# Optimization experiments

Hardware: AMD Instinct MI355X
Metric: run time of the kernel (lower is better)

Reference implementation:

```python
import jax, jax.numpy as jnp
import numpy as np

N_NODES = 50000
D = 512
N_EDGES = 1600000

def setup_inputs() -> dict:
    key = jax.random.key(0)
    ks = jax.random.split(key, 5)
    x = jax.random.normal(ks[0], (N_NODES, D), dtype=jnp.float32)
    W = jax.random.normal(ks[1], (D, D), dtype=jnp.float32) * (1.0 / np.sqrt(D))
    b = jnp.zeros((D,), dtype=jnp.float32)
    edge_weight = jax.random.uniform(ks[2], (N_EDGES,), dtype=jnp.float32)
    edge_src = jax.random.randint(ks[3], (N_EDGES,), 0, N_NODES, dtype=jnp.int32)
    edge_dst = jax.random.randint(ks[4], (N_EDGES,), 0, N_NODES, dtype=jnp.int32)
    return {"x": x, "W": W, "b": b, "edge_weight": edge_weight,
            "edge_src": edge_src, "edge_dst": edge_dst}

def reference(x, W, b, edge_weight, edge_src, edge_dst):
    # GraphConvolution: support = x @ W; out = spmm(adj, support) + b
    support = x @ W                                  # [N, D] dense GEMM
    msgs = support[edge_src] * edge_weight[:, None]  # gather + scale [E, D]
    agg = jax.ops.segment_sum(msgs, edge_dst, num_segments=x.shape[0])  # [N, D]
    gc_out = agg + b
    # GCN2: relu then residual
    return jax.nn.relu(gc_out) + x
```

## Files before the change

### kernel.cpp

```cpp
#include <hip/hip_runtime.h>

#define N_NODES 50000
#define DIM 512
#define KCAT 1024
#define N_EDGES 1600000
#define CAP 96

typedef __attribute__((ext_vector_type(8))) short short8;
typedef __attribute__((ext_vector_type(8))) unsigned short ushort8;
typedef __attribute__((ext_vector_type(4))) float floatx4;
typedef __attribute__((ext_vector_type(2))) unsigned int uintx2;

__device__ __forceinline__ unsigned short f2bf(float v) {
    unsigned u = __float_as_uint(v);
    unsigned r = u + 0x7FFF + ((u >> 16) & 1);
    return (unsigned short)(r >> 16);
}
__device__ __forceinline__ float bf2f(unsigned short h) {
    return __uint_as_float((unsigned)h << 16);
}
__device__ __forceinline__ void stage16(const char* g, char* l) {
    __builtin_amdgcn_global_load_lds((const __attribute__((address_space(1))) void*)g,
                                     (__attribute__((address_space(3))) void*)l, 16, 0, 0);
}

__global__ __launch_bounds__(256) void convert_x(const float* __restrict__ x,
                                                 unsigned short* __restrict__ xcat) {
    const int t = blockIdx.x * 256 + threadIdx.x;
    if (t >= N_NODES * 64) return;
    const int row = t >> 6;
    const int kc = t & 63;
    const int blk = kc >> 3;
    const int c = kc & 7;
    const int cSw = c ^ (row & 7);

    const floatx4 v0 = __builtin_nontemporal_load((const floatx4*)&x[row * DIM + kc * 8]);
    const floatx4 v1 = __builtin_nontemporal_load((const floatx4*)&x[row * DIM + kc * 8 + 4]);
    float v[8] = {v0.x, v0.y, v0.z, v0.w, v1.x, v1.y, v1.z, v1.w};
    unsigned short h[8], l[8];
#pragma unroll
    for (int j = 0; j < 8; j++) {
        h[j] = f2bf(v[j]);
        l[j] = f2bf(v[j] - bf2f(h[j]));
    }
    const int o = row * KCAT + blk * 64 + cSw * 8;
    *(short8*)&xcat[o] = *(short8*)h;
    *(short8*)&xcat[o + DIM] = *(short8*)l;
}

__global__ __launch_bounds__(256) void convert_w(const float* __restrict__ W,
                                                 unsigned short* __restrict__ wcat) {
    const int t = blockIdx.x * 256 + threadIdx.x;
    if (t >= DIM * 64) return;
    const int n = t >> 6;
    const int kc = t & 63;
    const int blk = kc >> 3;
    const int c = kc & 7;
    const int cSw = c ^ (n & 7);

    unsigned short h[8];
#pragma unroll
    for (int j = 0; j < 8; j++) h[j] = f2bf(W[(kc * 8 + j) * DIM + n]);
    const int o = n * KCAT + blk * 64 + cSw * 8;
    *(short8*)&wcat[o] = *(short8*)h;
    *(short8*)&wcat[o + DIM] = *(short8*)h;
}

__global__ __launch_bounds__(256, 3) void gemm_cat(const unsigned short* __restrict__ A,
                                                   const unsigned short* __restrict__ B,
                                                   unsigned short* __restrict__ Cb, int M) {
    __shared__ __align__(128) char smem[32768];

    const int tid = threadIdx.x;
    const int row0 = blockIdx.y * 128;
    const int col0 = blockIdx.x * 128;

    int srow[4], schk[4];
#pragma unroll
    for (int i = 0; i < 4; i++) {
        const int q = i * 256 + tid;
        srow[i] = q >> 3;
        schk[i] = q & 7;
    }

    const int l = tid & 63;
    const int w = tid >> 6;
    const int wm = w & 1, wn = w >> 1;
    const int lrow = l & 15;
    const int kg = l >> 4;
    const int s = l & 7;

    int offA[4][2], offB[4][2];
#pragma unroll
    for (int mt = 0; mt < 4; mt++)
#pragma unroll
        for (int h = 0; h < 2; h++) {
            const int chunk = (kg + 4 * h) ^ s;
            offA[mt][h] = (wm * 64 + mt * 16 + lrow) * 128 + chunk * 16;
            offB[mt][h] = 16384 + (wn * 64 + mt * 16 + lrow) * 128 + chunk * 16;
        }

    floatx4 acc[4][4];
#pragma unroll
    for (int i = 0; i < 4; i++)
#pragma unroll
        for (int j = 0; j < 4; j++) acc[i][j] = (floatx4)(0.f);

    const char* A8 = (const char*)A;
    const char* B8 = (const char*)B;

    for (int kblk = 0; kblk < 16; kblk++) {
        __syncthreads();
#pragma unroll
        for (int i = 0; i < 4; i++) {
            const int q16 = (i * 256 + tid) * 16;
            const size_t ga = (size_t)min(row0 + srow[i], M - 1) * (KCAT * 2)
                              + kblk * 128 + schk[i] * 16;
            const size_t gb = (size_t)(col0 + srow[i]) * (KCAT * 2)
                              + kblk * 128 + schk[i] * 16;
            stage16(A8 + ga, smem + q16);
            stage16(B8 + gb, smem + 16384 + q16);
        }
        __syncthreads();

#pragma unroll
        for (int h = 0; h < 2; h++) {
            short8 bf[4];
#pragma unroll
            for (int nt = 0; nt < 4; nt++) bf[nt] = *(const short8*)(smem + offB[nt][h]);
#pragma unroll
            for (int mt = 0; mt < 4; mt++) {
                const short8 af = *(const short8*)(smem + offA[mt][h]);
#pragma unroll
                for (int nt = 0; nt < 4; nt++)
                    acc[mt][nt] = __builtin_amdgcn_mfma_f32_16x16x32_bf16(
                        af, bf[nt], acc[mt][nt], 0, 0, 0);
            }
        }
    }

    const int crow0 = row0 + wm * 64;
    const int ccol0 = col0 + wn * 64;
#pragma unroll
    for (int mt = 0; mt < 4; mt++) {
        const int rbase = crow0 + mt * 16 + kg * 4;
#pragma unroll
        for (int nt = 0; nt < 4; nt++) {
            const int cc = ccol0 + nt * 16 + lrow;
#pragma unroll
            for (int r = 0; r < 4; r++) {
                const int gr = rbase + r;
                if (gr < M) Cb[(size_t)gr * DIM + cc] = f2bf(acc[mt][nt][r]);
            }
        }
    }
}

__global__ __launch_bounds__(256) void gcn_build_edges(const int* __restrict__ esrc,
                                                       const int* __restrict__ edst,
                                                       const float* __restrict__ ew,
                                                       int* __restrict__ cursor,
                                                       unsigned int* __restrict__ table) {
    const int e = blockIdx.x * 256 + threadIdx.x;
    if (e >= N_EDGES) return;
    const int d = __builtin_nontemporal_load(&edst[e]);
    const int s = __builtin_nontemporal_load(&esrc[e]);
    const float w = __builtin_nontemporal_load(&ew[e]);
    const int pos = atomicAdd(&cursor[d], 1);
    if (pos < CAP) {
        uintx2 pk;
        pk.x = (unsigned)s;
        pk.y = __float_as_uint(w);
        __builtin_nontemporal_store(pk, (uintx2*)&table[(size_t)(d * CAP + pos) * 2]);
    }
}

__global__ __launch_bounds__(64, 8) void gcn_aggregate(const unsigned short* __restrict__ sup,
                                                       const int* __restrict__ cursor,
                                                       const unsigned int* __restrict__ table,
                                                       const unsigned short* __restrict__ xcat,
                                                       const float* __restrict__ b,
                                                       float* __restrict__ out) {
    const int n = blockIdx.x;
    const int tid = threadIdx.x;
    const int c = tid * 8;

    __shared__ uintx2 s_e[CAP];
    const int deg = min(cursor[n], CAP);
    if (tid < deg)
        s_e[tid] = __builtin_nontemporal_load((const uintx2*)&table[(size_t)(n * CAP + tid) * 2]);
    if (tid + 64 < deg)
        s_e[tid + 64] = __builtin_nontemporal_load((const uintx2*)&table[(size_t)(n * CAP + tid + 64) * 2]);
    __syncthreads();

    float acc[8];
#pragma unroll
    for (int j = 0; j < 8; j++) acc[j] = 0.f;

    const unsigned short* supc = sup + c;

    int i = 0;
    for (; i + 8 <= deg; i += 8) {
        float wts[8];
        ushort8 v[8];
#pragma unroll
        for (int u = 0; u < 8; u++) {
            const uintx2 e = s_e[i + u];
            wts[u] = __uint_as_float(e.y);
            v[u] = *(const ushort8*)(supc + (size_t)e.x * DIM);
        }
#pragma unroll
        for (int u = 0; u < 8; u++)
#pragma unroll
            for (int j = 0; j < 8; j++) acc[j] = fmaf(wts[u], bf2f(v[u][j]), acc[j]);
    }
    for (; i < deg; i++) {
        const uintx2 e = s_e[i];
        const float wt = __uint_as_float(e.y);
        const ushort8 v = *(const ushort8*)(supc + (size_t)e.x * DIM);
#pragma unroll
        for (int j = 0; j < 8; j++) acc[j] = fmaf(wt, bf2f(v[j]), acc[j]);
    }

    const int xoff = n * KCAT + (tid >> 3) * 64 + (((tid & 7) ^ (n & 7)) * 8);
    const ushort8 xb = __builtin_nontemporal_load((const ushort8*)&xcat[xoff]);
    const float4 b0 = *(const float4*)&b[c];
    const float4 b1 = *(const float4*)&b[c + 4];
    const float bb[8] = {b0.x, b0.y, b0.z, b0.w, b1.x, b1.y, b1.z, b1.w};
    floatx4 o0, o1;
    float o[8];
#pragma unroll
    for (int j = 0; j < 8; j++) o[j] = fmaxf(acc[j] + bb[j], 0.f) + bf2f(xb[j]);
    o0.x = o[0]; o0.y = o[1]; o0.z = o[2]; o0.w = o[3];
    o1.x = o[4]; o1.y = o[5]; o1.z = o[6]; o1.w = o[7];
    __builtin_nontemporal_store(o0, (floatx4*)&out[n * DIM + c]);
    __builtin_nontemporal_store(o1, (floatx4*)&out[n * DIM + c + 4]);
}

extern "C" void kernel_launch(void* const* d_in, const int* in_sizes, int n_in,
                              void* d_out, int out_size, void* d_ws, size_t ws_size,
                              hipStream_t stream) {
    const float* x = (const float*)d_in[0];
    const float* W = (const float*)d_in[1];
    const float* b = (const float*)d_in[2];
    const float* ew = (const float*)d_in[3];
    const int* esrc = (const int*)d_in[4];
    const int* edst = (const int*)d_in[5];
    float* out = (float*)d_out;

    char* ws = (char*)d_ws;
    size_t off = 0;
    unsigned short* support = (unsigned short*)(ws + off); off += (size_t)N_NODES * DIM * 2;
    int* cursor = (int*)(ws + off);                   off += (size_t)N_NODES * 4;
    unsigned int* table = (unsigned int*)(ws + off);  off += (size_t)N_NODES * CAP * 8;
    unsigned short* xcat = (unsigned short*)(ws + off); off += (size_t)N_NODES * KCAT * 2;
    unsigned short* wcat = (unsigned short*)(ws + off); off += (size_t)DIM * KCAT * 2;

    (void)hipMemsetAsync(cursor, 0, (size_t)N_NODES * sizeof(int), stream);

    convert_w<<<(DIM * 64 + 255) / 256, 256, 0, stream>>>(W, wcat);
    convert_x<<<(N_NODES * 64 + 255) / 256, 256, 0, stream>>>(x, xcat);

    gcn_build_edges<<<(N_EDGES + 255) / 256, 256, 0, stream>>>(esrc, edst, ew,
                                                               cursor, table);

    dim3 gemm_grid(DIM / 128, (N_NODES + 127) / 128);
    gemm_cat<<<gemm_grid, 256, 0, stream>>>(xcat, wcat, support, N_NODES);

    gcn_aggregate<<<N_NODES, 64, 0, stream>>>(support, cursor, table, xcat, b, out);
}
```

Before: 645.2 us.

## Bucket edges by source chunk and aggregate eight destinations per block

Replaces the single atomic edge-bucketing pass with a count, prefix and scatter sequence. Edges are now ordered within each destination by source chunk of 2048 nodes. The aggregation kernel handles eight destination nodes per 64-thread block and walks the chunks in order, so gathers of support rows from the same source range happen close together in time, aiming for better cache reuse. In exchange it adds an extra pass over the edges and a larger bounds array to clear, and the inner gather loop is no longer unrolled, which leaves fewer independent loads in flight per wave. CAP also drops from 96 to 80, which raises the risk of dropping edges at high-degree nodes.

```diff
diff --git a/kernel.cpp b/kernel.cpp
--- a/kernel.cpp
+++ b/kernel.cpp
@@ -4,7 +4,10 @@
 #define DIM 512
 #define KCAT 1024
 #define N_EDGES 1600000
-#define CAP 96
+#define CAP 80
+#define CHSHIFT 11
+#define NCHUNK 25
+#define DPW 8
 
 typedef __attribute__((ext_vector_type(8))) short short8;
 typedef __attribute__((ext_vector_type(8))) unsigned short ushort8;
@@ -156,17 +159,39 @@
     }
 }
 
-__global__ __launch_bounds__(256) void gcn_build_edges(const int* __restrict__ esrc,
-                                                       const int* __restrict__ edst,
-                                                       const float* __restrict__ ew,
-                                                       int* __restrict__ cursor,
-                                                       unsigned int* __restrict__ table) {
+__global__ __launch_bounds__(256) void gcn_count(const int* __restrict__ esrc,
+                                                 const int* __restrict__ edst,
+                                                 int* __restrict__ bounds) {
     const int e = blockIdx.x * 256 + threadIdx.x;
     if (e >= N_EDGES) return;
+    const int s = __builtin_nontemporal_load(&esrc[e]);
     const int d = __builtin_nontemporal_load(&edst[e]);
+    atomicAdd(&bounds[(s >> CHSHIFT) * N_NODES + d], 1);
+}
+
+__global__ __launch_bounds__(256) void gcn_prefix(int* __restrict__ bounds) {
+    const int dst = blockIdx.x * 256 + threadIdx.x;
+    if (dst >= N_NODES) return;
+    int run = 0;
+#pragma unroll
+    for (int c = 0; c < NCHUNK; c++) {
+        const int t = bounds[c * N_NODES + dst];
+        bounds[c * N_NODES + dst] = run;
+        run += t;
+    }
+}
+
+__global__ __launch_bounds__(256) void gcn_scatter(const int* __restrict__ esrc,
+                                                   const int* __restrict__ edst,
+                                                   const float* __restrict__ ew,
+                                                   int* __restrict__ bounds,
+                                                   unsigned int* __restrict__ table) {
+    const int e = blockIdx.x * 256 + threadIdx.x;
+    if (e >= N_EDGES) return;
     const int s = __builtin_nontemporal_load(&esrc[e]);
+    const int d = __builtin_nontemporal_load(&edst[e]);
     const float w = __builtin_nontemporal_load(&ew[e]);
-    const int pos = atomicAdd(&cursor[d], 1);
+    const int pos = atomicAdd(&bounds[(s >> CHSHIFT) * N_NODES + d], 1);
     if (pos < CAP) {
         uintx2 pk;
         pk.x = (unsigned)s;
@@ -175,66 +200,61 @@
     }
 }
 
-__global__ __launch_bounds__(64, 8) void gcn_aggregate(const unsigned short* __restrict__ sup,
-                                                       const int* __restrict__ cursor,
+__global__ __launch_bounds__(64, 4) void gcn_aggregate(const unsigned short* __restrict__ sup,
+                                                       const int* __restrict__ bounds,
                                                        const unsigned int* __restrict__ table,
                                                        const unsigned short* __restrict__ xcat,
                                                        const float* __restrict__ b,
                                                        float* __restrict__ out) {
-    const int n = blockIdx.x;
+    const int nb = blockIdx.x * DPW;
     const int tid = threadIdx.x;
-    const int c = tid * 8;
-
-    __shared__ uintx2 s_e[CAP];
-    const int deg = min(cursor[n], CAP);
-    if (tid < deg)
-        s_e[tid] = __builtin_nontemporal_load((const uintx2*)&table[(size_t)(n * CAP + tid) * 2]);
-    if (tid + 64 < deg)
-        s_e[tid + 64] = __builtin_nontemporal_load((const uintx2*)&table[(size_t)(n * CAP + tid + 64) * 2]);
-    __syncthreads();
-
-    float acc[8];
-#pragma unroll
-    for (int j = 0; j < 8; j++) acc[j] = 0.f;
-
-    const unsigned short* supc = sup + c;
-
-    int i = 0;
-    for (; i + 8 <= deg; i += 8) {
-        float wts[8];
-        ushort8 v[8];
-#pragma unroll
-        for (int u = 0; u < 8; u++) {
-            const uintx2 e = s_e[i + u];
-            wts[u] = __uint_as_float(e.y);
-            v[u] = *(const ushort8*)(supc + (size_t)e.x * DIM);
-        }
-#pragma unroll
-        for (int u = 0; u < 8; u++)
-#pragma unroll
-            for (int j = 0; j < 8; j++) acc[j] = fmaf(wts[u], bf2f(v[u][j]), acc[j]);
-    }
-    for (; i < deg; i++) {
-        const uintx2 e = s_e[i];
-        const float wt = __uint_as_float(e.y);
-        const ushort8 v = *(const ushort8*)(supc + (size_t)e.x * DIM);
-#pragma unroll
-        for (int j = 0; j < 8; j++) acc[j] = fmaf(wt, bf2f(v[j]), acc[j]);
-    }
-
-    const int xoff = n * KCAT + (tid >> 3) * 64 + (((tid & 7) ^ (n & 7)) * 8);
-    const ushort8 xb = __builtin_nontemporal_load((const ushort8*)&xcat[xoff]);
-    const float4 b0 = *(const float4*)&b[c];
-    const float4 b1 = *(const float4*)&b[c + 4];
+    const int c8 = tid * 8;
+
+    float acc[DPW][8];
+#pragma unroll
+    for (int d = 0; d < DPW; d++)
+#pragma unroll
+        for (int j = 0; j < 8; j++) acc[d][j] = 0.f;
+
+    int prevEnd[DPW];
+#pragma unroll
+    for (int d = 0; d < DPW; d++) prevEnd[d] = 0;
+
+    const unsigned short* supc = sup + c8;
+
+    for (int c = 0; c < NCHUNK; c++) {
+#pragma unroll
+        for (int d = 0; d < DPW; d++) {
+            const int dst = nb + d;
+            const int end = min(bounds[c * N_NODES + dst], CAP);
+            for (int i = prevEnd[d]; i < end; i++) {
+                const uintx2 e = *(const uintx2*)&table[(size_t)(dst * CAP + i) * 2];
+                const float wt = __uint_as_float(e.y);
+                const ushort8 v = *(const ushort8*)(supc + (size_t)e.x * DIM);
+#pragma unroll
+                for (int j = 0; j < 8; j++) acc[d][j] = fmaf(wt, bf2f(v[j]), acc[d][j]);
+            }
+            prevEnd[d] = end;
+        }
+    }
+
+    const float4 b0 = *(const float4*)&b[c8];
+    const float4 b1 = *(const float4*)&b[c8 + 4];
     const float bb[8] = {b0.x, b0.y, b0.z, b0.w, b1.x, b1.y, b1.z, b1.w};
-    floatx4 o0, o1;
-    float o[8];
-#pragma unroll
-    for (int j = 0; j < 8; j++) o[j] = fmaxf(acc[j] + bb[j], 0.f) + bf2f(xb[j]);
-    o0.x = o[0]; o0.y = o[1]; o0.z = o[2]; o0.w = o[3];
-    o1.x = o[4]; o1.y = o[5]; o1.z = o[6]; o1.w = o[7];
-    __builtin_nontemporal_store(o0, (floatx4*)&out[n * DIM + c]);
-    __builtin_nontemporal_store(o1, (floatx4*)&out[n * DIM + c + 4]);
+#pragma unroll
+    for (int d = 0; d < DPW; d++) {
+        const int n = nb + d;
+        const int xoff = n * KCAT + (tid >> 3) * 64 + (((tid & 7) ^ (n & 7)) * 8);
+        const ushort8 xb = __builtin_nontemporal_load((const ushort8*)&xcat[xoff]);
+        float o[8];
+#pragma unroll
+        for (int j = 0; j < 8; j++) o[j] = fmaxf(acc[d][j] + bb[j], 0.f) + bf2f(xb[j]);
+        floatx4 o0, o1;
+        o0.x = o[0]; o0.y = o[1]; o0.z = o[2]; o0.w = o[3];
+        o1.x = o[4]; o1.y = o[5]; o1.z = o[6]; o1.w = o[7];
+        __builtin_nontemporal_store(o0, (floatx4*)&out[(size_t)n * DIM + c8]);
+        __builtin_nontemporal_store(o1, (floatx4*)&out[(size_t)n * DIM + c8 + 4]);
+    }
 }
 
 extern "C" void kernel_launch(void* const* d_in, const int* in_sizes, int n_in,
@@ -251,21 +271,22 @@
     char* ws = (char*)d_ws;
     size_t off = 0;
     unsigned short* support = (unsigned short*)(ws + off); off += (size_t)N_NODES * DIM * 2;
-    int* cursor = (int*)(ws + off);                   off += (size_t)N_NODES * 4;
+    int* bounds = (int*)(ws + off);                   off += (size_t)NCHUNK * N_NODES * 4;
     unsigned int* table = (unsigned int*)(ws + off);  off += (size_t)N_NODES * CAP * 8;
     unsigned short* xcat = (unsigned short*)(ws + off); off += (size_t)N_NODES * KCAT * 2;
     unsigned short* wcat = (unsigned short*)(ws + off); off += (size_t)DIM * KCAT * 2;
 
-    (void)hipMemsetAsync(cursor, 0, (size_t)N_NODES * sizeof(int), stream);
+    (void)hipMemsetAsync(bounds, 0, (size_t)NCHUNK * N_NODES * sizeof(int), stream);
 
     convert_w<<<(DIM * 64 + 255) / 256, 256, 0, stream>>>(W, wcat);
     convert_x<<<(N_NODES * 64 + 255) / 256, 256, 0, stream>>>(x, xcat);
 
-    gcn_build_edges<<<(N_EDGES + 255) / 256, 256, 0, stream>>>(esrc, edst, ew,
-                                                               cursor, table);
+    gcn_count<<<(N_EDGES + 255) / 256, 256, 0, stream>>>(esrc, edst, bounds);
+    gcn_prefix<<<(N_NODES + 255) / 256, 256, 0, stream>>>(bounds);
+    gcn_scatter<<<(N_EDGES + 255) / 256, 256, 0, stream>>>(esrc, edst, ew, bounds, table);
 
     dim3 gemm_grid(DIM / 128, (N_NODES + 127) / 128);
     gemm_cat<<<gemm_grid, 256, 0, stream>>>(xcat, wcat, support, N_NODES);
 
-    gcn_aggregate<<<N_NODES, 64, 0, stream>>>(support, cursor, table, xcat, b, out);
-}
+    gcn_aggregate<<<N_NODES / DPW, 64, 0, stream>>>(support, bounds, table, xcat, b, out);
+}
```

Result: slower. 767.9 us (+19.0%).

## Sort per-node edge lists by source and stagger gather start for cache locality

Applied to the files above, without the earlier changes.

Each aggregation block now bitonic-sorts its edge list by source index in shared memory, then starts its gather at a source offset that depends on the node id and wraps around. The aim is for concurrently running blocks to touch similar regions of the support matrix at the same time, improving L2 hit rates for the random gathers. The cost is a 28-step shared-memory sort with a barrier per step, and the loop loses its batched 8-wide load unrolling, which reduces memory-level parallelism.

```diff
diff --git a/kernel.cpp b/kernel.cpp
--- a/kernel.cpp
+++ b/kernel.cpp
@@ -5,6 +5,7 @@
 #define KCAT 1024
 #define N_EDGES 1600000
 #define CAP 96
+#define GEN 6400
 
 typedef __attribute__((ext_vector_type(8))) short short8;
 typedef __attribute__((ext_vector_type(8))) unsigned short ushort8;
@@ -175,57 +176,75 @@
     }
 }
 
-__global__ __launch_bounds__(64, 8) void gcn_aggregate(const unsigned short* __restrict__ sup,
-                                                       const int* __restrict__ cursor,
-                                                       const unsigned int* __restrict__ table,
-                                                       const unsigned short* __restrict__ xcat,
-                                                       const float* __restrict__ b,
-                                                       float* __restrict__ out) {
+__global__ __launch_bounds__(64) void gcn_aggregate(const unsigned short* __restrict__ sup,
+                                                    const int* __restrict__ cursor,
+                                                    const unsigned int* __restrict__ table,
+                                                    const unsigned short* __restrict__ xcat,
+                                                    const float* __restrict__ b,
+                                                    float* __restrict__ out) {
     const int n = blockIdx.x;
     const int tid = threadIdx.x;
-    const int c = tid * 8;
-
-    __shared__ uintx2 s_e[CAP];
+    const int c8 = tid * 8;
+
+    __shared__ uintx2 s_e[128];
     const int deg = min(cursor[n], CAP);
-    if (tid < deg)
-        s_e[tid] = __builtin_nontemporal_load((const uintx2*)&table[(size_t)(n * CAP + tid) * 2]);
-    if (tid + 64 < deg)
-        s_e[tid + 64] = __builtin_nontemporal_load((const uintx2*)&table[(size_t)(n * CAP + tid + 64) * 2]);
+
+    uintx2 pad; pad.x = 0xFFFFFFFFu; pad.y = 0;
+    s_e[tid] = (tid < deg)
+        ? *(const uintx2*)&table[(size_t)(n * CAP + tid) * 2] : pad;
+    s_e[tid + 64] = (tid + 64 < deg)
+        ? *(const uintx2*)&table[(size_t)(n * CAP + tid + 64) * 2] : pad;
     __syncthreads();
 
+#pragma unroll
+    for (int k = 2; k <= 128; k <<= 1) {
+        for (int j = k >> 1; j > 0; j >>= 1) {
+            const int i = ((tid & ~(j - 1)) << 1) | (tid & (j - 1));
+            const int p = i | j;
+            const uintx2 a = s_e[i];
+            const uintx2 q = s_e[p];
+            const bool up = (i & k) == 0;
+            const bool sw = up ? (a.x > q.x) : (a.x < q.x);
+            if (sw) { s_e[i] = q; s_e[p] = a; }
+            __syncthreads();
+        }
+    }
+
+    const unsigned s0 =
+        (unsigned)(((unsigned long long)(n % GEN) * N_NODES) / GEN);
+    const unsigned long long m0 = __ballot(s_e[tid].x >= s0);
+    const unsigned long long m1 = __ballot(s_e[tid + 64].x >= s0);
+    int start = m0 ? (__ffsll((long long)m0) - 1)
+                   : (m1 ? 64 + __ffsll((long long)m1) - 1 : 128);
+    start = min(start, deg);
+
     float acc[8];
 #pragma unroll
     for (int j = 0; j < 8; j++) acc[j] = 0.f;
 
-    const unsigned short* supc = sup + c;
-
-    int i = 0;
-    for (; i + 8 <= deg; i += 8) {
-        float wts[8];
-        ushort8 v[8];
-#pragma unroll
-        for (int u = 0; u < 8; u++) {
-            const uintx2 e = s_e[i + u];
-            wts[u] = __uint_as_float(e.y);
-            v[u] = *(const ushort8*)(supc + (size_t)e.x * DIM);
-        }
-#pragma unroll
-        for (int u = 0; u < 8; u++)
-#pragma unroll
-            for (int j = 0; j < 8; j++) acc[j] = fmaf(wts[u], bf2f(v[u][j]), acc[j]);
-    }
-    for (; i < deg; i++) {
+    const unsigned short* supc = sup + c8;
+
+#pragma unroll 4
+    for (int i = start; i < deg; i++) {
         const uintx2 e = s_e[i];
         const float wt = __uint_as_float(e.y);
         const ushort8 v = *(const ushort8*)(supc + (size_t)e.x * DIM);
 #pragma unroll
         for (int j = 0; j < 8; j++) acc[j] = fmaf(wt, bf2f(v[j]), acc[j]);
     }
+#pragma unroll 4
+    for (int i = 0; i < start; i++) {
+        const uintx2 e = s_e[i];
+        const float wt = __uint_as_float(e.y);
+        const ushort8 v = *(const ushort8*)(supc + (size_t)e.x * DIM);
+#pragma unroll
+        for (int j = 0; j < 8; j++) acc[j] = fmaf(wt, bf2f(v[j]), acc[j]);
+    }
 
     const int xoff = n * KCAT + (tid >> 3) * 64 + (((tid & 7) ^ (n & 7)) * 8);
     const ushort8 xb = __builtin_nontemporal_load((const ushort8*)&xcat[xoff]);
-    const float4 b0 = *(const float4*)&b[c];
-    const float4 b1 = *(const float4*)&b[c + 4];
+    const float4 b0 = *(const float4*)&b[c8];
+    const float4 b1 = *(const float4*)&b[c8 + 4];
     const float bb[8] = {b0.x, b0.y, b0.z, b0.w, b1.x, b1.y, b1.z, b1.w};
     floatx4 o0, o1;
     float o[8];
@@ -233,8 +252,8 @@
     for (int j = 0; j < 8; j++) o[j] = fmaxf(acc[j] + bb[j], 0.f) + bf2f(xb[j]);
     o0.x = o[0]; o0.y = o[1]; o0.z = o[2]; o0.w = o[3];
     o1.x = o[4]; o1.y = o[5]; o1.z = o[6]; o1.w = o[7];
-    __builtin_nontemporal_store(o0, (floatx4*)&out[n * DIM + c]);
-    __builtin_nontemporal_store(o1, (floatx4*)&out[n * DIM + c + 4]);
+    __builtin_nontemporal_store(o0, (floatx4*)&out[n * DIM + c8]);
+    __builtin_nontemporal_store(o1, (floatx4*)&out[n * DIM + c8 + 4]);
 }
 
 extern "C" void kernel_launch(void* const* d_in, const int* in_sizes, int n_in,
```

New measurement: 631.3 us. 2.2% less time.

## Bucket edges by source chunk and sweep chunks across destinations in persistent aggregate

Applied to the files above, without the earlier changes.

Edges are now binned per destination into four source-index chunks (by src>>14), each capped at 40 slots. A persistent aggregate kernel gives each wave 12 destination nodes and walks chunk by chunk across all of them. At any moment the gathered support rows come from one quarter of the node range, which should improve L2 hit rate on the random gathers. A tail kernel handles the leftover nodes. In exchange, each wave holds 96 float accumulators per lane with lower occupancy, the edge list is no longer staged in LDS, and per-chunk caps could drop edges for skewed degree distributions.

```diff
diff --git a/kernel.cpp b/kernel.cpp
--- a/kernel.cpp
+++ b/kernel.cpp
@@ -4,7 +4,11 @@
 #define DIM 512
 #define KCAT 1024
 #define N_EDGES 1600000
-#define CAP 96
+#define NCHUNK 4
+#define CAPC 40
+#define PBLK 4096
+#define DPW 12
+#define TAIL (N_NODES - PBLK * DPW)
 
 typedef __attribute__((ext_vector_type(8))) short short8;
 typedef __attribute__((ext_vector_type(8))) unsigned short ushort8;
@@ -166,75 +170,112 @@
     const int d = __builtin_nontemporal_load(&edst[e]);
     const int s = __builtin_nontemporal_load(&esrc[e]);
     const float w = __builtin_nontemporal_load(&ew[e]);
-    const int pos = atomicAdd(&cursor[d], 1);
-    if (pos < CAP) {
+    const int ch = s >> 14;
+    const int pos = atomicAdd(&cursor[ch * N_NODES + d], 1);
+    if (pos < CAPC) {
         uintx2 pk;
         pk.x = (unsigned)s;
         pk.y = __float_as_uint(w);
-        __builtin_nontemporal_store(pk, (uintx2*)&table[(size_t)(d * CAP + pos) * 2]);
-    }
-}
-
-__global__ __launch_bounds__(64, 8) void gcn_aggregate(const unsigned short* __restrict__ sup,
-                                                       const int* __restrict__ cursor,
-                                                       const unsigned int* __restrict__ table,
-                                                       const unsigned short* __restrict__ xcat,
-                                                       const float* __restrict__ b,
-                                                       float* __restrict__ out) {
-    const int n = blockIdx.x;
-    const int tid = threadIdx.x;
-    const int c = tid * 8;
-
-    __shared__ uintx2 s_e[CAP];
-    const int deg = min(cursor[n], CAP);
-    if (tid < deg)
-        s_e[tid] = __builtin_nontemporal_load((const uintx2*)&table[(size_t)(n * CAP + tid) * 2]);
-    if (tid + 64 < deg)
-        s_e[tid + 64] = __builtin_nontemporal_load((const uintx2*)&table[(size_t)(n * CAP + tid + 64) * 2]);
-    __syncthreads();
-
-    float acc[8];
-#pragma unroll
-    for (int j = 0; j < 8; j++) acc[j] = 0.f;
-
-    const unsigned short* supc = sup + c;
-
-    int i = 0;
-    for (; i + 8 <= deg; i += 8) {
-        float wts[8];
-        ushort8 v[8];
-#pragma unroll
-        for (int u = 0; u < 8; u++) {
-            const uintx2 e = s_e[i + u];
-            wts[u] = __uint_as_float(e.y);
-            v[u] = *(const ushort8*)(supc + (size_t)e.x * DIM);
-        }
-#pragma unroll
-        for (int u = 0; u < 8; u++)
-#pragma unroll
-            for (int j = 0; j < 8; j++) acc[j] = fmaf(wts[u], bf2f(v[u][j]), acc[j]);
-    }
-    for (; i < deg; i++) {
-        const uintx2 e = s_e[i];
-        const float wt = __uint_as_float(e.y);
-        const ushort8 v = *(const ushort8*)(supc + (size_t)e.x * DIM);
-#pragma unroll
-        for (int j = 0; j < 8; j++) acc[j] = fmaf(wt, bf2f(v[j]), acc[j]);
-    }
-
+        __builtin_nontemporal_store(
+            pk, (uintx2*)&table[(((size_t)d * NCHUNK + ch) * CAPC + pos) * 2]);
+    }
+}
+
+__device__ __forceinline__ void write_node(int n, int tid, const float* acc,
+                                           const float* bb,
+                                           const unsigned short* __restrict__ xcat,
+                                           float* __restrict__ out) {
+    const int c8 = tid * 8;
     const int xoff = n * KCAT + (tid >> 3) * 64 + (((tid & 7) ^ (n & 7)) * 8);
     const ushort8 xb = __builtin_nontemporal_load((const ushort8*)&xcat[xoff]);
-    const float4 b0 = *(const float4*)&b[c];
-    const float4 b1 = *(const float4*)&b[c + 4];
-    const float bb[8] = {b0.x, b0.y, b0.z, b0.w, b1.x, b1.y, b1.z, b1.w};
+    float o[8];
+#pragma unroll
+    for (int j = 0; j < 8; j++) o[j] = fmaxf(acc[j] + bb[j], 0.f) + bf2f(xb[j]);
     floatx4 o0, o1;
-    float o[8];
-#pragma unroll
-    for (int j = 0; j < 8; j++) o[j] = fmaxf(acc[j] + bb[j], 0.f) + bf2f(xb[j]);
     o0.x = o[0]; o0.y = o[1]; o0.z = o[2]; o0.w = o[3];
     o1.x = o[4]; o1.y = o[5]; o1.z = o[6]; o1.w = o[7];
-    __builtin_nontemporal_store(o0, (floatx4*)&out[n * DIM + c]);
-    __builtin_nontemporal_store(o1, (floatx4*)&out[n * DIM + c + 4]);
+    __builtin_nontemporal_store(o0, (floatx4*)&out[(size_t)n * DIM + c8]);
+    __builtin_nontemporal_store(o1, (floatx4*)&out[(size_t)n * DIM + c8 + 4]);
+}
+
+__global__ __launch_bounds__(64, 4) void gcn_aggregate_pers(
+        const unsigned short* __restrict__ sup,
+        const int* __restrict__ cursor,
+        const unsigned int* __restrict__ table,
+        const unsigned short* __restrict__ xcat,
+        const float* __restrict__ b,
+        float* __restrict__ out) {
+    const int w = blockIdx.x;
+    const int tid = threadIdx.x;
+    const int c8 = tid * 8;
+
+    float acc[DPW][8];
+#pragma unroll
+    for (int k = 0; k < DPW; k++)
+#pragma unroll
+        for (int j = 0; j < 8; j++) acc[k][j] = 0.f;
+
+    const unsigned short* supc = sup + c8;
+
+    for (int c = 0; c < NCHUNK; c++) {
+#pragma unroll
+        for (int k = 0; k < DPW; k++) {
+            const int dst = w + k * PBLK;
+            const int cnt = min(cursor[c * N_NODES + dst], CAPC);
+            const size_t segbase = ((size_t)dst * NCHUNK + c) * CAPC;
+#pragma unroll 2
+            for (int i = 0; i < cnt; i++) {
+                const uintx2 e = *(const uintx2*)&table[(segbase + i) * 2];
+                const float wt = __uint_as_float(e.y);
+                const ushort8 v = *(const ushort8*)(supc + (size_t)e.x * DIM);
+#pragma unroll
+                for (int j = 0; j < 8; j++) acc[k][j] = fmaf(wt, bf2f(v[j]), acc[k][j]);
+            }
+        }
+    }
+
+    const float4 b0 = *(const float4*)&b[c8];
+    const float4 b1 = *(const float4*)&b[c8 + 4];
+    const float bb[8] = {b0.x, b0.y, b0.z, b0.w, b1.x, b1.y, b1.z, b1.w};
+#pragma unroll
+    for (int k = 0; k < DPW; k++)
+        write_node(w + k * PBLK, tid, acc[k], bb, xcat, out);
+}
+
+__global__ __launch_bounds__(64) void gcn_aggregate_tail(
+        const unsigned short* __restrict__ sup,
+        const int* __restrict__ cursor,
+        const unsigned int* __restrict__ table,
+        const unsigned short* __restrict__ xcat,
+        const float* __restrict__ b,
+        float* __restrict__ out) {
+    const int n = PBLK * DPW + blockIdx.x;
+    const int tid = threadIdx.x;
+    const int c8 = tid * 8;
+
+    float acc[8];
+#pragma unroll
+    for (int j = 0; j < 8; j++) acc[j] = 0.f;
+
+    const unsigned short* supc = sup + c8;
+
+    for (int c = 0; c < NCHUNK; c++) {
+        const int cnt = min(cursor[c * N_NODES + n], CAPC);
+        const size_t segbase = ((size_t)n * NCHUNK + c) * CAPC;
+#pragma unroll 2
+        for (int i = 0; i < cnt; i++) {
+            const uintx2 e = *(const uintx2*)&table[(segbase + i) * 2];
+            const float wt = __uint_as_float(e.y);
+            const ushort8 v = *(const ushort8*)(supc + (size_t)e.x * DIM);
+#pragma unroll
+            for (int j = 0; j < 8; j++) acc[j] = fmaf(wt, bf2f(v[j]), acc[j]);
+        }
+    }
+
+    const float4 b0 = *(const float4*)&b[c8];
+    const float4 b1 = *(const float4*)&b[c8 + 4];
+    const float bb[8] = {b0.x, b0.y, b0.z, b0.w, b1.x, b1.y, b1.z, b1.w};
+    write_node(n, tid, acc, bb, xcat, out);
 }
 
 extern "C" void kernel_launch(void* const* d_in, const int* in_sizes, int n_in,
@@ -251,12 +292,12 @@
     char* ws = (char*)d_ws;
     size_t off = 0;
     unsigned short* support = (unsigned short*)(ws + off); off += (size_t)N_NODES * DIM * 2;
-    int* cursor = (int*)(ws + off);                   off += (size_t)N_NODES * 4;
-    unsigned int* table = (unsigned int*)(ws + off);  off += (size_t)N_NODES * CAP * 8;
+    int* cursor = (int*)(ws + off);                   off += (size_t)NCHUNK * N_NODES * 4;
+    unsigned int* table = (unsigned int*)(ws + off);  off += (size_t)N_NODES * NCHUNK * CAPC * 8;
     unsigned short* xcat = (unsigned short*)(ws + off); off += (size_t)N_NODES * KCAT * 2;
     unsigned short* wcat = (unsigned short*)(ws + off); off += (size_t)DIM * KCAT * 2;
 
-    (void)hipMemsetAsync(cursor, 0, (size_t)N_NODES * sizeof(int), stream);
+    (void)hipMemsetAsync(cursor, 0, (size_t)NCHUNK * N_NODES * sizeof(int), stream);
 
     convert_w<<<(DIM * 64 + 255) / 256, 256, 0, stream>>>(W, wcat);
     convert_x<<<(N_NODES * 64 + 255) / 256, 256, 0, stream>>>(x, xcat);
@@ -267,5 +308,6 @@
     dim3 gemm_grid(DIM / 128, (N_NODES + 127) / 128);
     gemm_cat<<<gemm_grid, 256, 0, stream>>>(xcat, wcat, support, N_NODES);
 
-    gcn_aggregate<<<N_NODES, 64, 0, stream>>>(support, cursor, table, xcat, b, out);
-}
+    gcn_aggregate_pers<<<PBLK, 64, 0, stream>>>(support, cursor, table, xcat, b, out);
+    gcn_aggregate_tail<<<TAIL, 64, 0, stream>>>(support, cursor, table, xcat, b, out);
+}
```

New measurement: 610.8 us. 5.3% less time.
